# Optimization experiments

Measured on AMD Instinct MI355X. Metric: run time of the kernel, lower is better.

Reference implementation:

```python
import jax, jax.numpy as jnp
import numpy as np

N = 100000
E = 1600000
IN_DIM = 128
H = 64
OUT_DIM = 64
EPS = 1e-5


def batch_norm(x, gamma, beta):
    # BatchNorm1d with batch statistics (training-mode normalization, biased var)
    mu = jnp.mean(x, axis=0)
    var = jnp.var(x, axis=0)
    return (x - mu) * jax.lax.rsqrt(var + EPS) * gamma + beta


def gcn_conv(x, src, dst, W, b, n_nodes):
    # PyG GCNConv: add self-loops, symmetric deg^-1/2 normalization, X W, scatter-add, bias
    loop = jnp.arange(n_nodes, dtype=src.dtype)
    s = jnp.concatenate([src, loop])
    d = jnp.concatenate([dst, loop])
    w = jnp.ones(s.shape[0], dtype=x.dtype)
    deg = jax.ops.segment_sum(w, d, num_segments=n_nodes)
    dinv = jnp.where(deg > 0, jax.lax.rsqrt(deg), 0.0)
    norm = dinv[s] * w * dinv[d]                      # [E+N]
    h = x @ W                                         # [N, out]
    msg = h[s] * norm[:, None]                        # [E+N, out]
    out = jax.ops.segment_sum(msg, d, num_segments=n_nodes)
    return out + b


def setup_inputs() -> dict:
    key = jax.random.key(0)
    ks = jax.random.split(key, 12)
    x = jax.random.normal(ks[0], (N, IN_DIM), dtype=jnp.float32)
    edge_index = jax.random.randint(ks[1], (2, E), 0, N, dtype=jnp.int64)
    s = 0.05
    return {
        "x": x,
        "edge_index": edge_index,
        "bn_in_g": jnp.ones((IN_DIM,), jnp.float32),
        "bn_in_b": jnp.zeros((IN_DIM,), jnp.float32),
        "Wp": jax.random.normal(ks[2], (IN_DIM, H), jnp.float32) * s,
        "bp": jnp.zeros((H,), jnp.float32),
        "W1": jax.random.normal(ks[3], (H, H), jnp.float32) * s,
        "b1": jnp.zeros((H,), jnp.float32),
        "bn1_g": jnp.ones((H,), jnp.float32),
        "bn1_b": jnp.zeros((H,), jnp.float32),
        "W2": jax.random.normal(ks[4], (H, OUT_DIM), jnp.float32) * s,
        "b2": jnp.zeros((OUT_DIM,), jnp.float32),
        "bn2_g": jnp.ones((OUT_DIM,), jnp.float32),
        "bn2_b": jnp.zeros((OUT_DIM,), jnp.float32),
    }


def reference(x, edge_index, bn_in_g, bn_in_b, Wp, bp, W1, b1, bn1_g, bn1_b, W2, b2, bn2_g, bn2_b):
    src, dst = edge_index[0], edge_index[1]
    n = x.shape[0]
    h0 = batch_norm(x, bn_in_g, bn_in_b)
    h0 = jax.nn.relu(h0 @ Wp + bp)
    h1 = gcn_conv(h0, src, dst, W1, b1, n)
    h1 = jax.nn.relu(batch_norm(h1, bn1_g, bn1_b))
    # dropout in eval mode: identity
    h2 = gcn_conv(h1, src, dst, W2, b2, n)
    return batch_norm(h2, bn2_g, bn2_b)
```

## Files before the change

### kernel.cpp

```cpp
#include <hip/hip_runtime.h>
#include <hip/hip_bf16.h>

#define EPS 1e-5f
#define CAP 6144
#define PCHUNK 4096
#define XP 68

__device__ __forceinline__ void acc_q(float* acc, uint2 v, float s) {
    acc[0] += s * (float)((int)(v.x << 24) >> 24);
    acc[1] += s * (float)((int)(v.x << 16) >> 24);
    acc[2] += s * (float)((int)(v.x << 8) >> 24);
    acc[3] += s * (float)((int)v.x >> 24);
    acc[4] += s * (float)((int)(v.y << 24) >> 24);
    acc[5] += s * (float)((int)(v.y << 16) >> 24);
    acc[6] += s * (float)((int)(v.y << 8) >> 24);
    acc[7] += s * (float)((int)v.y >> 24);
}

#define GEMM_KK(kk, wvec)                                                        \
    {                                                                            \
        float a0 = (kk == 0) ? xv0.x : (kk == 1) ? xv0.y : (kk == 2) ? xv0.z : xv0.w; \
        float a1 = (kk == 0) ? xv1.x : (kk == 1) ? xv1.y : (kk == 2) ? xv1.z : xv1.w; \
        float a2 = (kk == 0) ? xv2.x : (kk == 1) ? xv2.y : (kk == 2) ? xv2.z : xv2.w; \
        float a3 = (kk == 0) ? xv3.x : (kk == 1) ? xv3.y : (kk == 2) ? xv3.z : xv3.w; \
        acc[0][0] += a0 * wvec.x; acc[0][1] += a0 * wvec.y;                      \
        acc[0][2] += a0 * wvec.z; acc[0][3] += a0 * wvec.w;                      \
        acc[1][0] += a1 * wvec.x; acc[1][1] += a1 * wvec.y;                      \
        acc[1][2] += a1 * wvec.z; acc[1][3] += a1 * wvec.w;                      \
        acc[2][0] += a2 * wvec.x; acc[2][1] += a2 * wvec.y;                      \
        acc[2][2] += a2 * wvec.z; acc[2][3] += a2 * wvec.w;                      \
        acc[3][0] += a3 * wvec.x; acc[3][1] += a3 * wvec.y;                      \
        acc[3][2] += a3 * wvec.z; acc[3][3] += a3 * wvec.w;                      \
    }

__global__ void k_init(int* __restrict__ cur, float* __restrict__ stats) {
    int t = threadIdx.x;
    stats[t] = 0.0f;
    cur[t] = t * CAP;
}

__global__ __launch_bounds__(256) void k_A(
    const int* __restrict__ src, const int* __restrict__ dst,
    int* __restrict__ cur, unsigned* __restrict__ packbuf, int E, int NBP,
    const float* __restrict__ x, float* __restrict__ xsum, float* __restrict__ xsq, int N) {
    __shared__ int h[512], delta[512], wsc[4];
    __shared__ unsigned buf[PCHUNK];
    __shared__ int addr[PCHUNK];
    int tx = threadIdx.x;
    if ((int)blockIdx.x < NBP) {
        int e0 = blockIdx.x * PCHUNK;
        int e1 = min(e0 + PCHUNK, E);
        int csize = e1 - e0;
        h[tx] = 0; h[tx + 256] = 0;
        __syncthreads();
        for (int e = e0 + tx; e < e1; e += 256)
            atomicAdd(&h[dst[e] >> 8], 1);
        __syncthreads();
        int b0 = tx * 2;
        int c0 = h[b0], c1 = h[b0 + 1];
        int tsum = c0 + c1;
        int lane = tx & 63, wid = tx >> 6;
        int v = tsum;
#pragma unroll
        for (int off = 1; off < 64; off <<= 1) {
            int u = __shfl_up(v, off);
            if (lane >= off) v += u;
        }
        if (lane == 63) wsc[wid] = v;
        __syncthreads();
        int wbase = 0;
        for (int w = 0; w < wid; w++) wbase += wsc[w];
        int excl0 = wbase + v - tsum;
        int excl1 = excl0 + c0;
        if (c0 > 0) delta[b0] = atomicAdd(&cur[b0], c0) - excl0;
        if (c1 > 0) delta[b0 + 1] = atomicAdd(&cur[b0 + 1], c1) - excl1;
        __syncthreads();
        h[b0] = excl0; h[b0 + 1] = excl1;
        __syncthreads();
        for (int e = e0 + tx; e < e1; e += 256) {
            int d = dst[e];
            int b = d >> 8;
            int rank = atomicAdd(&h[b], 1);
            buf[rank] = ((unsigned)src[e] << 8) | (unsigned)(d & 255);
            addr[rank] = delta[b];
        }
        __syncthreads();
        for (int i = tx; i < csize; i += 256)
            packbuf[addr[i] + i] = buf[i];
    } else {
        float* ls = (float*)buf;
        float* lq = ls + 256;
        int b2 = blockIdx.x - NBP;
        int col = tx & 127, half = tx >> 7;
        float s = 0.f, q = 0.f;
        for (int r = b2 * 2 + half; r < N; r += 1024) {
            float v = x[(long long)r * 128 + col];
            s += v; q += v * v;
        }
        ls[tx] = s; lq[tx] = q;
        __syncthreads();
        if (half == 0) {
            s = ls[tx] + ls[tx + 128];
            q = lq[tx] + lq[tx + 128];
            atomicAdd(&xsum[col], s);
            atomicAdd(&xsq[col], q);
        }
    }
}

__global__ __launch_bounds__(512) void k_B(
    const unsigned* __restrict__ packbuf, const int* __restrict__ cur,
    int2* __restrict__ rowbe, int* __restrict__ rowmid, float* __restrict__ dinv,
    int* __restrict__ eidx, int NB, int N, int Nh,
    const float* __restrict__ x, const float* __restrict__ stats,
    const float* __restrict__ g, const float* __restrict__ bbn,
    const float* __restrict__ Wp, const float* __restrict__ bp,
    const float* __restrict__ W1, unsigned* __restrict__ Bq, float* __restrict__ S,
    float invN) {
    __shared__ __align__(16) char smem[52224];
    int tx = threadIdx.x;
    if ((int)blockIdx.x < NB) {
        int* cnt  = (int*)smem;
        int* loff = cnt + 512;
        int* wsum = loff + 512;
        int b = blockIdx.x;
        int base = b * CAP;
        int end = cur[b];
        cnt[tx] = 0;
        __syncthreads();
        for (int e = base + tx; e < end; e += 512) {
            unsigned pk = packbuf[e];
            int key = (((int)pk & 255) << 1) | (int)((pk >> 8) >= (unsigned)Nh);
            atomicAdd(&cnt[key], 1);
        }
        __syncthreads();
        int c = cnt[tx];
        int lane = tx & 63, wid = tx >> 6;
        int v = c;
#pragma unroll
        for (int off = 1; off < 64; off <<= 1) {
            int u = __shfl_up(v, off);
            if (lane >= off) v += u;
        }
        if (lane == 63) wsum[wid] = v;
        __syncthreads();
        int wbase = 0;
        for (int w = 0; w < wid; w++) wbase += wsum[w];
        int excl = wbase + v - c;
        loff[tx] = excl;
        __syncthreads();
        if (tx < 256) {
            int node = b * 256 + tx;
            if (node < N) {
                int beg = base + loff[2 * tx];
                int mid = base + loff[2 * tx + 1];
                int e2 = mid + cnt[2 * tx + 1];
                rowbe[node] = make_int2(beg, e2);
                rowmid[node] = mid;
                int deg = cnt[2 * tx] + cnt[2 * tx + 1];
                dinv[node] = rsqrtf(1.0f + (float)deg);
            }
        }
        __syncthreads();
        for (int e = base + tx; e < end; e += 512) {
            unsigned pk = packbuf[e];
            int key = (((int)pk & 255) << 1) | (int)((pk >> 8) >= (unsigned)Nh);
            int pos = atomicAdd(&loff[key], 1);
            eidx[base + pos] = (int)(pk >> 8);
        }
    } else {
        float* xs  = (float*)smem;
        float* ws  = xs + 128 * XP;
        float* scb = ws + 4096;
        float* shb = scb + 128;
        if (tx < 128) {
            float mu = stats[tx] * invN;
            float var = stats[128 + tx] * invN - mu * mu;
            float s = g[tx] * rsqrtf(var + EPS);
            scb[tx] = s;
            shb[tx] = bbn[tx] - mu * s;
        }
        __syncthreads();
        int r0 = ((int)blockIdx.x - NB) * 128;
        int cw = tx & 15, rw = tx >> 4;
        float acc[4][4];
#pragma unroll
        for (int j = 0; j < 4; j++)
#pragma unroll
            for (int i = 0; i < 4; i++) acc[j][i] = 0.f;

#pragma unroll 1
        for (int kc = 0; kc < 128; kc += 64) {
#pragma unroll
            for (int i = 0; i < 4; i++) {
                int f = tx + 512 * i;
                int row = f >> 4, kq = f & 15;
                int rr = r0 + row;
                float4 v = make_float4(0.f, 0.f, 0.f, 0.f);
                if (rr < N) v = ((const float4*)(x + (long long)rr * 128 + kc))[kq];
                int cb = kc + kq * 4;
                v.x = v.x * scb[cb + 0] + shb[cb + 0];
                v.y = v.y * scb[cb + 1] + shb[cb + 1];
                v.z = v.z * scb[cb + 2] + shb[cb + 2];
                v.w = v.w * scb[cb + 3] + shb[cb + 3];
                *(float4*)&xs[row * XP + kq * 4] = v;
            }
#pragma unroll
            for (int i = 0; i < 2; i++) {
                int f = tx + 512 * i;
                int k = f >> 4, cq = f & 15;
                float4 w = ((const float4*)(Wp + (long long)(kc + k) * 64))[cq];
                *(float4*)&ws[k * 64 + cq * 4] = w;
            }
            __syncthreads();
#pragma unroll 1
            for (int k4 = 0; k4 < 16; k4++) {
                float4 xv0 = *(const float4*)&xs[(rw * 4 + 0) * XP + k4 * 4];
                float4 xv1 = *(const float4*)&xs[(rw * 4 + 1) * XP + k4 * 4];
                float4 xv2 = *(const float4*)&xs[(rw * 4 + 2) * XP + k4 * 4];
                float4 xv3 = *(const float4*)&xs[(rw * 4 + 3) * XP + k4 * 4];
#pragma unroll
                for (int kk = 0; kk < 4; kk++) {
                    float4 w = *(const float4*)&ws[(k4 * 4 + kk) * 64 + cw * 4];
                    GEMM_KK(kk, w);
                }
            }
            __syncthreads();
        }
        float4 bpv = ((const float4*)bp)[cw];
#pragma unroll
        for (int j = 0; j < 4; j++) {
            float4 o;
            o.x = fmaxf(acc[j][0] + bpv.x, 0.f);
            o.y = fmaxf(acc[j][1] + bpv.y, 0.f);
            o.z = fmaxf(acc[j][2] + bpv.z, 0.f);
            o.w = fmaxf(acc[j][3] + bpv.w, 0.f);
            *(float4*)&xs[(rw * 4 + j) * XP + cw * 4] = o;
        }
#pragma unroll
        for (int i = 0; i < 2; i++) {
            int f = tx + 512 * i;
            int k = f >> 4, cq = f & 15;
            float4 w = ((const float4*)(W1 + (long long)k * 64))[cq];
            *(float4*)&ws[k * 64 + cq * 4] = w;
        }
        __syncthreads();
#pragma unroll
        for (int j = 0; j < 4; j++)
#pragma unroll
            for (int i = 0; i < 4; i++) acc[j][i] = 0.f;
#pragma unroll 1
        for (int k4 = 0; k4 < 16; k4++) {
            float4 xv0 = *(const float4*)&xs[(rw * 4 + 0) * XP + k4 * 4];
            float4 xv1 = *(const float4*)&xs[(rw * 4 + 1) * XP + k4 * 4];
            float4 xv2 = *(const float4*)&xs[(rw * 4 + 2) * XP + k4 * 4];
            float4 xv3 = *(const float4*)&xs[(rw * 4 + 3) * XP + k4 * 4];
#pragma unroll
            for (int kk = 0; kk < 4; kk++) {
                float4 w = *(const float4*)&ws[(k4 * 4 + kk) * 64 + cw * 4];
                GEMM_KK(kk, w);
            }
        }
#pragma unroll
        for (int j = 0; j < 4; j++) {
            int rr = r0 + rw * 4 + j;
            float m = 0.f;
#pragma unroll
            for (int i = 0; i < 4; i++) m = fmaxf(m, fabsf(acc[j][i]));
#pragma unroll
            for (int mask = 1; mask < 16; mask <<= 1)
                m = fmaxf(m, __shfl_xor(m, mask, 64));
            float inv = (m > 0.f) ? (127.0f / m) : 0.f;
            if (rr < N) {
                if (cw == 0) S[rr] = m * (1.0f / 127.0f);
                int q0 = (int)rintf(acc[j][0] * inv);
                int q1 = (int)rintf(acc[j][1] * inv);
                int q2 = (int)rintf(acc[j][2] * inv);
                int q3 = (int)rintf(acc[j][3] * inv);
                unsigned w = ((unsigned)q0 & 255u) | (((unsigned)q1 & 255u) << 8) |
                             (((unsigned)q2 & 255u) << 16) | (((unsigned)q3 & 255u) << 24);
                Bq[(long long)rr * 16 + cw] = w;
            }
        }
    }
}

__global__ __launch_bounds__(256) void k_scale(float* __restrict__ S,
                                               const float* __restrict__ dinv, int N) {
    int r = blockIdx.x * 256 + threadIdx.x;
    if (r < N) S[r] *= dinv[r];
}

template <bool BNRELU>
__global__ __launch_bounds__(512) void k_gemm_scale(
    const float* __restrict__ In, const float* __restrict__ W,
    const float* __restrict__ dinv, const float* __restrict__ ssum,
    const float* __restrict__ ssq, const float* __restrict__ g,
    const float* __restrict__ bb, float invN, unsigned* __restrict__ Bq,
    float* __restrict__ S, int N) {
    __shared__ __align__(16) char smem[52224];
    float* xs  = (float*)smem;
    float* ws  = xs + 128 * XP;
    float* scb = ws + 4096;
    float* shb = scb + 128;
    int tx = threadIdx.x;
    if (BNRELU) {
        if (tx < 64) {
            float mu = ssum[tx] * invN;
            float var = ssq[tx] * invN - mu * mu;
            float s = g[tx] * rsqrtf(var + EPS);
            scb[tx] = s;
            shb[tx] = bb[tx] - mu * s;
        }
        __syncthreads();
    }
    int r0 = blockIdx.x * 128;
    int cw = tx & 15, rw = tx >> 4;
#pragma unroll
    for (int i = 0; i < 4; i++) {
        int f = tx + 512 * i;
        int row = f >> 4, kq = f & 15;
        int rr = r0 + row;
        float4 v = make_float4(0.f, 0.f, 0.f, 0.f);
        if (rr < N) v = ((const float4*)(In + (long long)rr * 64))[kq];
        if (BNRELU) {
            int cb = kq * 4;
            v.x = fmaxf(v.x * scb[cb + 0] + shb[cb + 0], 0.f);
            v.y = fmaxf(v.y * scb[cb + 1] + shb[cb + 1], 0.f);
            v.z = fmaxf(v.z * scb[cb + 2] + shb[cb + 2], 0.f);
            v.w = fmaxf(v.w * scb[cb + 3] + shb[cb + 3], 0.f);
        }
        *(float4*)&xs[row * XP + kq * 4] = v;
    }
#pragma unroll
    for (int i = 0; i < 2; i++) {
        int f = tx + 512 * i;
        int k = f >> 4, cq = f & 15;
        float4 w = ((const float4*)(W + (long long)k * 64))[cq];
        *(float4*)&ws[k * 64 + cq * 4] = w;
    }
    __syncthreads();
    float acc[4][4];
#pragma unroll
    for (int j = 0; j < 4; j++)
#pragma unroll
        for (int i = 0; i < 4; i++) acc[j][i] = 0.f;
#pragma unroll 1
    for (int k4 = 0; k4 < 16; k4++) {
        float4 xv0 = *(const float4*)&xs[(rw * 4 + 0) * XP + k4 * 4];
        float4 xv1 = *(const float4*)&xs[(rw * 4 + 1) * XP + k4 * 4];
        float4 xv2 = *(const float4*)&xs[(rw * 4 + 2) * XP + k4 * 4];
        float4 xv3 = *(const float4*)&xs[(rw * 4 + 3) * XP + k4 * 4];
#pragma unroll
        for (int kk = 0; kk < 4; kk++) {
            float4 w = *(const float4*)&ws[(k4 * 4 + kk) * 64 + cw * 4];
            GEMM_KK(kk, w);
        }
    }
#pragma unroll
    for (int j = 0; j < 4; j++) {
        int rr = r0 + rw * 4 + j;
        float dv = (rr < N) ? dinv[rr] : 0.f;
        float m = 0.f;
#pragma unroll
        for (int i = 0; i < 4; i++) {
            acc[j][i] *= dv;
            m = fmaxf(m, fabsf(acc[j][i]));
        }
#pragma unroll
        for (int mask = 1; mask < 16; mask <<= 1)
            m = fmaxf(m, __shfl_xor(m, mask, 64));
        float inv = (m > 0.f) ? (127.0f / m) : 0.f;
        if (rr < N) {
            if (cw == 0) S[rr] = m * (1.0f / 127.0f);
            int q0 = (int)rintf(acc[j][0] * inv);
            int q1 = (int)rintf(acc[j][1] * inv);
            int q2 = (int)rintf(acc[j][2] * inv);
            int q3 = (int)rintf(acc[j][3] * inv);
            unsigned w = ((unsigned)q0 & 255u) | (((unsigned)q1 & 255u) << 8) |
                         (((unsigned)q2 & 255u) << 16) | (((unsigned)q3 & 255u) << 24);
            Bq[(long long)rr * 16 + cw] = w;
        }
    }
}

__global__ __launch_bounds__(256) void k_gather_finish(
    const uint2* __restrict__ Q, const float* __restrict__ S,
    const int2* __restrict__ rowbe, const int* __restrict__ rowmid,
    const int* __restrict__ eidx,
    const float* __restrict__ dinv, const float* __restrict__ bias,
    float* __restrict__ Out, float* __restrict__ ssum, float* __restrict__ ssq,
    int N, int Nh) {
    int tx = threadIdx.x;
    int g = tx >> 3;
    int l = tx & 7;
    int d = blockIdx.x * 32 + g;

    float s[8], q[8];
#pragma unroll
    for (int j = 0; j < 8; j++) { s[j] = 0.f; q[j] = 0.f; }

    if (d < N) {
        int2 be = rowbe[d];
        int mid = rowmid[d];
        uint2 v0 = Q[(long long)d * 8 + l];
        float sd = S[d];
        float dv = dinv[d];

        float acc[8];
#pragma unroll
        for (int j = 0; j < 8; j++) acc[j] = 0.f;

        for (int seg = 0; seg < 2; seg++) {
            int k  = seg ? mid : be.x;
            int ke = seg ? be.y : mid;
            if (k >= ke) continue;
            int dmy = seg ? Nh : 0;
            int idx_cur[8];
#pragma unroll
            for (int j = 0; j < 8; j++)
                idx_cur[j] = (k + j < ke) ? eidx[k + j] : dmy;

            while (k < ke) {
                uint2 bb[8];
                float sv[8];
#pragma unroll
                for (int j = 0; j < 8; j++)
                    bb[j] = Q[(long long)idx_cur[j] * 8 + l];
#pragma unroll
                for (int j = 0; j < 8; j++)
                    sv[j] = (k + j < ke) ? S[idx_cur[j]] : 0.f;
                int kn = k + 8;
                int idx_nxt[8];
#pragma unroll
                for (int j = 0; j < 8; j++)
                    idx_nxt[j] = (kn + j < ke) ? eidx[kn + j] : dmy;
#pragma unroll
                for (int j = 0; j < 8; j++)
                    acc_q(acc, bb[j], sv[j]);
#pragma unroll
                for (int j = 0; j < 8; j++) idx_cur[j] = idx_nxt[j];
                k = kn;
            }
        }
        acc_q(acc, v0, sd);

        float4 o0, o1;
#pragma unroll
        for (int j = 0; j < 8; j++) {
            float v = acc[j] * dv + bias[8 * l + j];
            ((j < 4) ? (&o0.x)[j] : (&o1.x)[j - 4]) = v;
            s[j] += v; q[j] += v * v;
        }
        float4* outp = (float4*)(Out + (long long)d * 64 + 8 * l);
        outp[0] = o0;
        outp[1] = o1;
    }

#pragma unroll
    for (int m = 8; m <= 32; m <<= 1) {
#pragma unroll
        for (int j = 0; j < 8; j++) {
            s[j] += __shfl_xor(s[j], m, 64);
            q[j] += __shfl_xor(q[j], m, 64);
        }
    }
    __shared__ float ws_s[4][64], ws_q[4][64];
    int wv = tx >> 6, ln = tx & 63;
    if (ln < 8) {
#pragma unroll
        for (int j = 0; j < 8; j++) {
            ws_s[wv][ln * 8 + j] = s[j];
            ws_q[wv][ln * 8 + j] = q[j];
        }
    }
    __syncthreads();
    if (tx < 64) {
        float S2 = ws_s[0][tx] + ws_s[1][tx] + ws_s[2][tx] + ws_s[3][tx];
        float Q2 = ws_q[0][tx] + ws_q[1][tx] + ws_q[2][tx] + ws_q[3][tx];
        atomicAdd(&ssum[tx], S2);
        atomicAdd(&ssq[tx], Q2);
    }
}

__global__ __launch_bounds__(256) void k_final(const float* __restrict__ In,
                                               const float* __restrict__ ssum,
                                               const float* __restrict__ ssq,
                                               const float* __restrict__ g,
                                               const float* __restrict__ bb, float invN,
                                               float* __restrict__ out, int total4) {
    __shared__ float scs[64], shs[64];
    int tx = threadIdx.x;
    if (tx < 64) {
        float mu = ssum[tx] * invN;
        float var = ssq[tx] * invN - mu * mu;
        float s = g[tx] * rsqrtf(var + EPS);
        scs[tx] = s;
        shs[tx] = bb[tx] - mu * s;
    }
    __syncthreads();
    int t = blockIdx.x * blockDim.x + tx;
    if (t < total4) {
        float4 v = ((const float4*)In)[t];
        int j = (t * 4) & 63;
        v.x = v.x * scs[j + 0] + shs[j + 0];
        v.y = v.y * scs[j + 1] + shs[j + 1];
        v.z = v.z * scs[j + 2] + shs[j + 2];
        v.w = v.w * scs[j + 3] + shs[j + 3];
        ((float4*)out)[t] = v;
    }
}

extern "C" void kernel_launch(void* const* d_in, const int* in_sizes, int n_in,
                              void* d_out, int out_size, void* d_ws, size_t ws_size,
                              hipStream_t stream) {
    const float* x       = (const float*)d_in[0];
    const int*   ei      = (const int*)d_in[1];
    const float* bn_in_g = (const float*)d_in[2];
    const float* bn_in_b = (const float*)d_in[3];
    const float* Wp      = (const float*)d_in[4];
    const float* bp      = (const float*)d_in[5];
    const float* W1      = (const float*)d_in[6];
    const float* b1      = (const float*)d_in[7];
    const float* bn1_g   = (const float*)d_in[8];
    const float* bn1_b   = (const float*)d_in[9];
    const float* W2      = (const float*)d_in[10];
    const float* b2      = (const float*)d_in[11];
    const float* bn2_g   = (const float*)d_in[12];
    const float* bn2_b   = (const float*)d_in[13];

    int N = in_sizes[0] / 128;
    int E = in_sizes[1] / 2;
    const int* src = ei;
    const int* dst = ei + E;
    int Nh  = N >> 1;
    int NB  = (N + 255) >> 8;
    int NBP = (E + PCHUNK - 1) / PCHUNK;
    int ntg = (N + 127) / 128;

    long long Npad = ((long long)N + 128) & ~127LL;
    int*   cur    = (int*)d_ws;
    float* stats  = (float*)(cur + 512);
    int2*  rowbe  = (int2*)(stats + 512);
    float* dinv   = (float*)(rowbe + Npad);
    int*   rowmid = (int*)(dinv + Npad);
    float* S      = (float*)(rowmid + Npad);
    unsigned* packbuf = (unsigned*)(S + Npad);
    int*   eidx   = (int*)(packbuf + (long long)NB * CAP);
    unsigned* Bq  = (unsigned*)(eidx + (long long)NB * CAP);
    float* H      = (float*)d_out;

    int gb = (N + 31) / 32;
    float invN = 1.0f / (float)N;

    k_init<<<1, 512, 0, stream>>>(cur, stats);
    k_A<<<NBP + 512, 256, 0, stream>>>(src, dst, cur, packbuf, E, NBP,
                                       x, stats, stats + 128, N);
    k_B<<<NB + ntg, 512, 0, stream>>>(packbuf, cur, rowbe, rowmid, dinv, eidx, NB, N, Nh,
                                      x, stats, bn_in_g, bn_in_b, Wp, bp, W1, Bq, S, invN);
    k_scale<<<(N + 255) / 256, 256, 0, stream>>>(S, dinv, N);
    k_gather_finish<<<gb, 256, 0, stream>>>((const uint2*)Bq, S, rowbe, rowmid, eidx, dinv,
                                            b1, H, stats + 256, stats + 320, N, Nh);

    k_gemm_scale<true><<<ntg, 512, 0, stream>>>(H, W2, dinv, stats + 256, stats + 320,
                                                bn1_g, bn1_b, invN, Bq, S, N);
    k_gather_finish<<<gb, 256, 0, stream>>>((const uint2*)Bq, S, rowbe, rowmid, eidx, dinv,
                                            b2, H, stats + 384, stats + 448, N, Nh);

    k_final<<<(N * 16 + 255) / 256, 256, 0, stream>>>(H, stats + 384, stats + 448,
                                                      bn2_g, bn2_b, invN, H, N * 16);
}
```

Baseline: 430.2 us.

## Cache edge data in registers, vectorize input stats, replace init kernel with memset

The edge-partition and CSR-build phases now load dst/src (and packed entries) into registers once and reuse them for both the histogram pass and the scatter pass, so the global re-read in the second pass goes away. The input column-stats branch reads float4 rows with more row groups per block. The init kernel is replaced by a memset, with the bucket base offsets folded into the address math. The fixed register arrays cap edges per block (PCHUNK/256 and CAP/512) and raise register pressure.

```diff
diff --git a/kernel.cpp b/kernel.cpp
--- a/kernel.cpp
+++ b/kernel.cpp
@@ -33,12 +33,6 @@
         acc[3][2] += a3 * wvec.z; acc[3][3] += a3 * wvec.w;                      \
     }
 
-__global__ void k_init(int* __restrict__ cur, float* __restrict__ stats) {
-    int t = threadIdx.x;
-    stats[t] = 0.0f;
-    cur[t] = t * CAP;
-}
-
 __global__ __launch_bounds__(256) void k_A(
     const int* __restrict__ src, const int* __restrict__ dst,
     int* __restrict__ cur, unsigned* __restrict__ packbuf, int E, int NBP,
@@ -53,8 +47,15 @@
         int csize = e1 - e0;
         h[tx] = 0; h[tx + 256] = 0;
         __syncthreads();
-        for (int e = e0 + tx; e < e1; e += 256)
-            atomicAdd(&h[dst[e] >> 8], 1);
+        int dreg[16], sreg[16];
+#pragma unroll
+        for (int i = 0; i < 16; i++) {
+            int e = e0 + tx + 256 * i;
+            bool ok = e < e1;
+            dreg[i] = ok ? dst[e] : -1;
+            sreg[i] = ok ? src[e] : 0;
+            if (ok) atomicAdd(&h[dreg[i] >> 8], 1);
+        }
         __syncthreads();
         int b0 = tx * 2;
         int c0 = h[b0], c1 = h[b0 + 1];
@@ -72,38 +73,50 @@
         for (int w = 0; w < wid; w++) wbase += wsc[w];
         int excl0 = wbase + v - tsum;
         int excl1 = excl0 + c0;
-        if (c0 > 0) delta[b0] = atomicAdd(&cur[b0], c0) - excl0;
-        if (c1 > 0) delta[b0 + 1] = atomicAdd(&cur[b0 + 1], c1) - excl1;
+        if (c0 > 0) delta[b0] = b0 * CAP + atomicAdd(&cur[b0], c0) - excl0;
+        if (c1 > 0) delta[b0 + 1] = (b0 + 1) * CAP + atomicAdd(&cur[b0 + 1], c1) - excl1;
         __syncthreads();
         h[b0] = excl0; h[b0 + 1] = excl1;
         __syncthreads();
-        for (int e = e0 + tx; e < e1; e += 256) {
-            int d = dst[e];
-            int b = d >> 8;
-            int rank = atomicAdd(&h[b], 1);
-            buf[rank] = ((unsigned)src[e] << 8) | (unsigned)(d & 255);
-            addr[rank] = delta[b];
+#pragma unroll
+        for (int i = 0; i < 16; i++) {
+            int d = dreg[i];
+            if (d >= 0) {
+                int b = d >> 8;
+                int rank = atomicAdd(&h[b], 1);
+                buf[rank] = ((unsigned)sreg[i] << 8) | (unsigned)(d & 255);
+                addr[rank] = delta[b];
+            }
         }
         __syncthreads();
         for (int i = tx; i < csize; i += 256)
             packbuf[addr[i] + i] = buf[i];
     } else {
         float* ls = (float*)buf;
-        float* lq = ls + 256;
+        float* lq = ls + 1024;
         int b2 = blockIdx.x - NBP;
-        int col = tx & 127, half = tx >> 7;
-        float s = 0.f, q = 0.f;
-        for (int r = b2 * 2 + half; r < N; r += 1024) {
-            float v = x[(long long)r * 128 + col];
-            s += v; q += v * v;
-        }
-        ls[tx] = s; lq[tx] = q;
-        __syncthreads();
-        if (half == 0) {
-            s = ls[tx] + ls[tx + 128];
-            q = lq[tx] + lq[tx + 128];
-            atomicAdd(&xsum[col], s);
-            atomicAdd(&xsq[col], q);
+        int c4 = tx & 31, rg = tx >> 5;
+        float s0 = 0.f, s1 = 0.f, s2 = 0.f, s3 = 0.f;
+        float q0 = 0.f, q1 = 0.f, q2 = 0.f, q3 = 0.f;
+        for (int r = b2 * 8 + rg; r < N; r += 4096) {
+            float4 v = ((const float4*)(x + (long long)r * 128))[c4];
+            s0 += v.x; q0 += v.x * v.x;
+            s1 += v.y; q1 += v.y * v.y;
+            s2 += v.z; q2 += v.z * v.z;
+            s3 += v.w; q3 += v.w * v.w;
+        }
+        int cb = c4 * 4;
+        ls[rg * 128 + cb + 0] = s0; lq[rg * 128 + cb + 0] = q0;
+        ls[rg * 128 + cb + 1] = s1; lq[rg * 128 + cb + 1] = q1;
+        ls[rg * 128 + cb + 2] = s2; lq[rg * 128 + cb + 2] = q2;
+        ls[rg * 128 + cb + 3] = s3; lq[rg * 128 + cb + 3] = q3;
+        __syncthreads();
+        if (tx < 128) {
+            float ss = 0.f, qq = 0.f;
+#pragma unroll
+            for (int k = 0; k < 8; k++) { ss += ls[k * 128 + tx]; qq += lq[k * 128 + tx]; }
+            atomicAdd(&xsum[tx], ss);
+            atomicAdd(&xsq[tx], qq);
         }
     }
 }
@@ -125,13 +138,20 @@
         int* wsum = loff + 512;
         int b = blockIdx.x;
         int base = b * CAP;
-        int end = cur[b];
+        int end = base + cur[b];
         cnt[tx] = 0;
         __syncthreads();
-        for (int e = base + tx; e < end; e += 512) {
-            unsigned pk = packbuf[e];
-            int key = (((int)pk & 255) << 1) | (int)((pk >> 8) >= (unsigned)Nh);
-            atomicAdd(&cnt[key], 1);
+        unsigned pkreg[12];
+#pragma unroll
+        for (int i = 0; i < 12; i++) {
+            int e = base + tx + 512 * i;
+            bool ok = e < end;
+            unsigned pk = ok ? packbuf[e] : 0xffffffffu;
+            pkreg[i] = pk;
+            if (ok) {
+                int key = (((int)pk & 255) << 1) | (int)((pk >> 8) >= (unsigned)Nh);
+                atomicAdd(&cnt[key], 1);
+            }
         }
         __syncthreads();
         int c = cnt[tx];
@@ -162,11 +182,14 @@
             }
         }
         __syncthreads();
-        for (int e = base + tx; e < end; e += 512) {
-            unsigned pk = packbuf[e];
-            int key = (((int)pk & 255) << 1) | (int)((pk >> 8) >= (unsigned)Nh);
-            int pos = atomicAdd(&loff[key], 1);
-            eidx[base + pos] = (int)(pk >> 8);
+#pragma unroll
+        for (int i = 0; i < 12; i++) {
+            unsigned pk = pkreg[i];
+            if (pk != 0xffffffffu) {
+                int key = (((int)pk & 255) << 1) | (int)((pk >> 8) >= (unsigned)Nh);
+                int pos = atomicAdd(&loff[key], 1);
+                eidx[base + pos] = (int)(pk >> 8);
+            }
         }
     } else {
         float* xs  = (float*)smem;
@@ -553,7 +576,7 @@
     int gb = (N + 31) / 32;
     float invN = 1.0f / (float)N;
 
-    k_init<<<1, 512, 0, stream>>>(cur, stats);
+    hipMemsetAsync(d_ws, 0, 1024 * sizeof(int), stream);
     k_A<<<NBP + 512, 256, 0, stream>>>(src, dst, cur, packbuf, E, NBP,
                                        x, stats, stats + 128, N);
     k_B<<<NB + ntg, 512, 0, stream>>>(packbuf, cur, rowbe, rowmid, dinv, eidx, NB, N, Nh,
```

Measured after the change: 398.2 us. 1.08x faster.
